# Kernel optimization log

Hardware: AMD Instinct MI355X
Metric: run time of the kernel (lower is better)

Reference implementation:

```python
import jax, jax.numpy as jnp
import numpy as np

B, L, D = 4, 4096, 64

def setup_inputs() -> dict:
    key = jax.random.key(0)
    k1, k2, k3, k4 = jax.random.split(key, 4)
    return {
        "query": jax.random.normal(k1, (B, L, D), dtype=jnp.float32),
        "key": jax.random.normal(k2, (B, L, D), dtype=jnp.float32),
        "value": jax.random.normal(k3, (B, L, D), dtype=jnp.float32),
        "mask": jax.random.uniform(k4, (B, L, L), dtype=jnp.float32),
        "d_k": D,
    }

def reference(query, key, value, mask, d_k):
    # scores: [B, Lq, Lk] = Q @ K^T / sqrt(d_k), then multiplicative mask
    scale = 1.0 / jnp.sqrt(jnp.asarray(d_k, dtype=query.dtype))
    scores = jnp.einsum("bqd,bkd->bqk", query, key) * scale * mask
    attn = jax.nn.softmax(scores, axis=-1)  # row-wise over keys
    return jnp.einsum("bqk,bkd->bqd", attn, value)
```

## Files before the change

kernel.cpp:

```cpp
#include <hip/hip_runtime.h>
#include <hip/hip_bf16.h>
#include <stdint.h>
#include <stddef.h>

#define B_   4
#define L_   4096
#define D_   64
#define TK_  64
#define NKT  (L_/TK_)
#define NKH  (NKT/2)
#define TQ_  64
#define NQB  (L_/TQ_)
#define KROW 144
#define TILE_BYTES (TK_*KROW)

typedef __attribute__((ext_vector_type(8))) short bf16x8;
typedef __attribute__((ext_vector_type(4))) float f32x4;
typedef __attribute__((ext_vector_type(4))) unsigned short u16x4;

__device__ static inline unsigned short f2bf(float x) {
  union { __hip_bfloat16 h; unsigned short u; } cv;
  cv.h = __float2bfloat16(x);
  return cv.u;
}

__global__ __launch_bounds__(512) void attn_fused(
    const float* __restrict__ Q, const float* __restrict__ K,
    const float* __restrict__ V, const float* __restrict__ Mk,
    float* __restrict__ out) {
  __shared__ char Kbuf[2][2][TILE_BYTES];
  __shared__ char Vbuf[2][2][TILE_BYTES];
  __shared__ char Pbuf[8][16*KROW];

  const int idx = blockIdx.x;
  const int b   = (idx & 7) >> 1;
  const int qt  = ((idx >> 3) << 1) | (idx & 1);

  const int tid  = threadIdx.x;
  const int w    = tid >> 6;
  const int qw   = w & 3;
  const int half = w >> 2;
  const int lane = tid & 63;
  const int i16  = lane & 15;
  const int quad = lane >> 4;
  const int q0   = qt*TQ_ + qw*16;

  const int st = tid & 255;
  const int dq = st & 15;
  const int kq = st >> 4;

  const float cs = 0.125f * 1.44269504088896f;
  bf16x8 aq[2];
  {
    const float* qp = Q + ((size_t)b*L_ + q0 + i16)*D_ + quad*8;
#pragma unroll
    for (int ks=0; ks<2; ++ks) {
      const f32x4* p = (const f32x4*)(qp + ks*32);
      f32x4 x0 = p[0], x1 = p[1];
      bf16x8 v;
      for (int j=0;j<4;++j) v[j]   = (short)f2bf(x0[j]*cs);
      for (int j=0;j<4;++j) v[4+j] = (short)f2bf(x1[j]*cs);
      aq[ks] = v;
    }
  }

  const float* mbase = Mk + ((size_t)b*L_ + q0 + quad*4)*(size_t)L_
                          + half*(NKH*TK_) + 4*i16;
  const size_t krow0 = (size_t)b*L_ + (size_t)half*(NKH*TK_) + kq*4;
  const float* kbase = K + krow0*D_ + dq*4;
  const float* vbase = V + krow0*D_ + dq*4;

  f32x4 O[4];
#pragma unroll
  for (int t=0;t<4;++t) O[t] = (f32x4){0.f,0.f,0.f,0.f};
  float l_acc[4] = {0.f,0.f,0.f,0.f};
  f32x4 cmv[4], nmv[4];
  f32x4 kreg[4], vreg[4];

#pragma unroll
  for (int r=0;r<4;++r) {
    kreg[r] = *(const f32x4*)(kbase + (size_t)r*D_);
    vreg[r] = *(const f32x4*)(vbase + (size_t)r*D_);
    cmv[r]  = *(const f32x4*)(mbase + (size_t)r*L_);
  }
#pragma unroll
  for (int r=0;r<4;++r) nmv[r] = cmv[r];

  for (int kt=0; kt<NKH; ++kt) {
    const int buf = kt & 1;

    {
      char* kb = Kbuf[half][buf]; char* vb = Vbuf[half][buf];
#pragma unroll
      for (int r=0;r<4;++r) {
        u16x4 pk;
        for (int j=0;j<4;++j) pk[j] = f2bf(kreg[r][j]);
        *(u16x4*)(kb + (r*16+kq)*KROW + dq*8) = pk;
      }
#pragma unroll
      for (int e=0;e<4;++e) {
        u16x4 pv;
        for (int r=0;r<4;++r) pv[r] = f2bf(vreg[r][e]);
        *(u16x4*)(vb + (dq*4+e)*KROW + kq*8) = pv;
      }
    }
    __syncthreads();

    if (kt+1 < NKH) {
      const size_t roff = (size_t)(kt+1)*TK_*(size_t)D_;
      const size_t kc   = (size_t)(kt+1)*TK_;
#pragma unroll
      for (int r=0;r<4;++r) {
        kreg[r] = *(const f32x4*)(kbase + roff + (size_t)r*D_);
        vreg[r] = *(const f32x4*)(vbase + roff + (size_t)r*D_);
        nmv[r]  = *(const f32x4*)(mbase + (size_t)r*L_ + kc);
      }
    }

    f32x4 acc[4];
    const char* kb = Kbuf[half][buf];
#pragma unroll
    for (int t=0;t<4;++t) {
      acc[t] = (f32x4){0.f,0.f,0.f,0.f};
#pragma unroll
      for (int ks=0;ks<2;++ks) {
        bf16x8 bfr = *(const bf16x8*)(kb + (t*16+i16)*KROW + ks*64 + quad*16);
        acc[t] = __builtin_amdgcn_mfma_f32_16x16x32_bf16(aq[ks], bfr, acc[t], 0,0,0);
      }
    }

    float p[16]; float rs[4] = {0.f,0.f,0.f,0.f};
#pragma unroll
    for (int t=0;t<4;++t)
#pragma unroll
      for (int r=0;r<4;++r) {
        float v = __builtin_amdgcn_exp2f(acc[t][r] * cmv[r][t]);
        p[t*4+r] = v; rs[r] += v;
      }
#pragma unroll
    for (int r=0;r<4;++r) {
      float s = rs[r];
      s += __shfl_xor(s, 1); s += __shfl_xor(s, 2);
      s += __shfl_xor(s, 4); s += __shfl_xor(s, 8);
      l_acc[r] += s;
    }

    char* pb = Pbuf[w];
#pragma unroll
    for (int r=0;r<4;++r) {
      u16x4 pk;
      for (int t=0;t<4;++t) pk[t] = f2bf(p[t*4+r]);
      *(u16x4*)(pb + (quad*4+r)*KROW + i16*8) = pk;
    }

    const char* vb = Vbuf[half][buf];
#pragma unroll
    for (int ks=0;ks<2;++ks) {
      bf16x8 af = *(const bf16x8*)(pb + i16*KROW + ks*64 + quad*16);
#pragma unroll
      for (int dt=0;dt<4;++dt) {
        bf16x8 vf = *(const bf16x8*)(vb + (dt*16+i16)*KROW + ks*64 + quad*16);
        O[dt] = __builtin_amdgcn_mfma_f32_16x16x32_bf16(af, vf, O[dt], 0,0,0);
      }
    }

#pragma unroll
    for (int r=0;r<4;++r) cmv[r] = nmv[r];
  }

  float* Ol = (float*)&Kbuf[0][0][0];
  float* Ll = (float*)&Pbuf[0][0];
  __syncthreads();
  if (half == 1) {
#pragma unroll
    for (int t=0;t<4;++t)
      *(f32x4*)&Ol[((size_t)qw*64 + t*16 + i16)*20 + quad*4] = O[t];
    if (i16 == 0) {
#pragma unroll
      for (int r=0;r<4;++r) Ll[qw*16 + quad*4 + r] = l_acc[r];
    }
  }
  __syncthreads();
  if (half == 0) {
#pragma unroll
    for (int t=0;t<4;++t) {
      f32x4 op = *(const f32x4*)&Ol[((size_t)qw*64 + t*16 + i16)*20 + quad*4];
      O[t] += op;
    }
    float inv[4];
#pragma unroll
    for (int r=0;r<4;++r) inv[r] = 1.0f / (l_acc[r] + Ll[qw*16 + quad*4 + r]);
#pragma unroll
    for (int t=0;t<4;++t)
#pragma unroll
      for (int r=0;r<4;++r)
        out[((size_t)b*L_ + q0 + quad*4 + r)*D_ + t*16 + i16] = O[t][r]*inv[r];
  }
}

extern "C" void kernel_launch(void* const* d_in, const int* in_sizes, int n_in,
                              void* d_out, int out_size, void* d_ws, size_t ws_size,
                              hipStream_t stream) {
  const float* Q  = (const float*)d_in[0];
  const float* K  = (const float*)d_in[1];
  const float* V  = (const float*)d_in[2];
  const float* Mk = (const float*)d_in[3];
  (void)d_ws; (void)ws_size;

  attn_fused<<<B_*NQB, 512, 0, stream>>>(Q, K, V, Mk, (float*)d_out);
}
```

Baseline: 407.5 us.

## Pre-convert K/V to bf16 LDS-layout tiles and compute row sums via MFMA

```diff
diff --git a/kernel.cpp b/kernel.cpp
--- a/kernel.cpp
+++ b/kernel.cpp
@@ -24,10 +24,42 @@
   return cv.u;
 }
 
-__global__ __launch_bounds__(512) void attn_fused(
-    const float* __restrict__ Q, const float* __restrict__ K,
-    const float* __restrict__ V, const float* __restrict__ Mk,
-    float* __restrict__ out) {
+
+__global__ __launch_bounds__(256) void prep_kv(const float* __restrict__ K,
+                                               const float* __restrict__ V,
+                                               char* __restrict__ kws,
+                                               char* __restrict__ vws) {
+  const int blk = blockIdx.x;
+  const int kt  = blk & (NKT-1);
+  const int b   = blk >> 6;
+  const int t   = threadIdx.x;
+  const int kr  = t >> 2;
+  const int ds  = t & 3;
+  const size_t row = (size_t)b*L_ + (size_t)kt*TK_ + kr;
+  const f32x4* kp = (const f32x4*)(K + row*D_ + ds*16);
+  const f32x4* vp = (const f32x4*)(V + row*D_ + ds*16);
+  f32x4 kv[4], vv[4];
+  for (int s=0;s<4;++s){ kv[s]=kp[s]; vv[s]=vp[s]; }
+
+  bf16x8 lo, hi;
+  for (int s=0;s<2;++s) for (int j=0;j<4;++j) lo[s*4+j] = (short)f2bf(kv[s  ][j]);
+  for (int s=0;s<2;++s) for (int j=0;j<4;++j) hi[s*4+j] = (short)f2bf(kv[2+s][j]);
+  const int slot = (kr&3)*16 + (kr>>2);
+  char* kdst = kws + (size_t)blk*TILE_BYTES + slot*KROW + ds*32;
+  *(bf16x8*)(kdst)    = lo;
+  *(bf16x8*)(kdst+16) = hi;
+
+  char* vdst = vws + (size_t)blk*TILE_BYTES + kr*2;
+  for (int s=0;s<4;++s)
+    for (int j=0;j<4;++j)
+      *(unsigned short*)(vdst + (size_t)(ds*16 + s*4 + j)*KROW) = f2bf(vv[s][j]);
+}
+
+__global__ __launch_bounds__(512) void attn_main(const float* __restrict__ Q,
+                                                 const float* __restrict__ Mk,
+                                                 const char* __restrict__ kws,
+                                                 const char* __restrict__ vws,
+                                                 float* __restrict__ out) {
   __shared__ char Kbuf[2][2][TILE_BYTES];
   __shared__ char Vbuf[2][2][TILE_BYTES];
   __shared__ char Pbuf[8][16*KROW];
@@ -45,10 +77,6 @@
   const int quad = lane >> 4;
   const int q0   = qt*TQ_ + qw*16;
 
-  const int st = tid & 255;
-  const int dq = st & 15;
-  const int kq = st >> 4;
-
   const float cs = 0.125f * 1.44269504088896f;
   bf16x8 aq[2];
   {
@@ -64,57 +92,66 @@
     }
   }
 
+  bf16x8 vone;
+#pragma unroll
+  for (int j=0;j<8;++j) vone[j] = (short)0x3F80;
+
   const float* mbase = Mk + ((size_t)b*L_ + q0 + quad*4)*(size_t)L_
                           + half*(NKH*TK_) + 4*i16;
-  const size_t krow0 = (size_t)b*L_ + (size_t)half*(NKH*TK_) + kq*4;
-  const float* kbase = K + krow0*D_ + dq*4;
-  const float* vbase = V + krow0*D_ + dq*4;
 
   f32x4 O[4];
 #pragma unroll
   for (int t=0;t<4;++t) O[t] = (f32x4){0.f,0.f,0.f,0.f};
-  float l_acc[4] = {0.f,0.f,0.f,0.f};
+  f32x4 l4 = (f32x4){0.f,0.f,0.f,0.f};
   f32x4 cmv[4], nmv[4];
-  f32x4 kreg[4], vreg[4];
-
-#pragma unroll
-  for (int r=0;r<4;++r) {
-    kreg[r] = *(const f32x4*)(kbase + (size_t)r*D_);
-    vreg[r] = *(const f32x4*)(vbase + (size_t)r*D_);
-    cmv[r]  = *(const f32x4*)(mbase + (size_t)r*L_);
-  }
+  bf16x8 sreg[5];
+
+  const size_t tb0 = (size_t)(b*NKT + half*NKH)*TILE_BYTES;
+
+#pragma unroll
+  for (int j=0;j<5;++j) {
+    const int c = qw + j*4;
+    if (c < 18) {
+      const char* gsrc = (c < 9)
+          ? (kws + tb0 + (size_t)c*1024)
+          : (vws + tb0 + (size_t)(c-9)*1024);
+      sreg[j] = *(const bf16x8*)(gsrc + lane*16);
+    }
+  }
+#pragma unroll
+  for (int r=0;r<4;++r) cmv[r] = *(const f32x4*)(mbase + (size_t)r*L_);
 #pragma unroll
   for (int r=0;r<4;++r) nmv[r] = cmv[r];
 
   for (int kt=0; kt<NKH; ++kt) {
     const int buf = kt & 1;
 
-    {
-      char* kb = Kbuf[half][buf]; char* vb = Vbuf[half][buf];
-#pragma unroll
-      for (int r=0;r<4;++r) {
-        u16x4 pk;
-        for (int j=0;j<4;++j) pk[j] = f2bf(kreg[r][j]);
-        *(u16x4*)(kb + (r*16+kq)*KROW + dq*8) = pk;
+#pragma unroll
+    for (int j=0;j<5;++j) {
+      const int c = qw + j*4;
+      if (c < 18) {
+        char* ldst = (c < 9) ? &Kbuf[half][buf][c*1024]
+                             : &Vbuf[half][buf][(c-9)*1024];
+        *(bf16x8*)(ldst + lane*16) = sreg[j];
       }
-#pragma unroll
-      for (int e=0;e<4;++e) {
-        u16x4 pv;
-        for (int r=0;r<4;++r) pv[r] = f2bf(vreg[r][e]);
-        *(u16x4*)(vb + (dq*4+e)*KROW + kq*8) = pv;
+    }
+    __syncthreads();
+
+    if (kt+1 < NKH) {
+      const size_t toff = tb0 + (size_t)(kt+1)*TILE_BYTES;
+#pragma unroll
+      for (int j=0;j<5;++j) {
+        const int c = qw + j*4;
+        if (c < 18) {
+          const char* gsrc = (c < 9)
+              ? (kws + toff + (size_t)c*1024)
+              : (vws + toff + (size_t)(c-9)*1024);
+          sreg[j] = *(const bf16x8*)(gsrc + lane*16);
+        }
       }
-    }
-    __syncthreads();
-
-    if (kt+1 < NKH) {
-      const size_t roff = (size_t)(kt+1)*TK_*(size_t)D_;
-      const size_t kc   = (size_t)(kt+1)*TK_;
-#pragma unroll
-      for (int r=0;r<4;++r) {
-        kreg[r] = *(const f32x4*)(kbase + roff + (size_t)r*D_);
-        vreg[r] = *(const f32x4*)(vbase + roff + (size_t)r*D_);
-        nmv[r]  = *(const f32x4*)(mbase + (size_t)r*L_ + kc);
-      }
+      const size_t kc = (size_t)(kt+1)*TK_;
+#pragma unroll
+      for (int r=0;r<4;++r) nmv[r] = *(const f32x4*)(mbase + (size_t)r*L_ + kc);
     }
 
     f32x4 acc[4];
@@ -129,21 +166,12 @@
       }
     }
 
-    float p[16]; float rs[4] = {0.f,0.f,0.f,0.f};
+    float p[16];
 #pragma unroll
     for (int t=0;t<4;++t)
 #pragma unroll
-      for (int r=0;r<4;++r) {
-        float v = __builtin_amdgcn_exp2f(acc[t][r] * cmv[r][t]);
-        p[t*4+r] = v; rs[r] += v;
-      }
-#pragma unroll
-    for (int r=0;r<4;++r) {
-      float s = rs[r];
-      s += __shfl_xor(s, 1); s += __shfl_xor(s, 2);
-      s += __shfl_xor(s, 4); s += __shfl_xor(s, 8);
-      l_acc[r] += s;
-    }
+      for (int r=0;r<4;++r)
+        p[t*4+r] = __builtin_amdgcn_exp2f(acc[t][r] * cmv[r][t]);
 
     char* pb = Pbuf[w];
 #pragma unroll
@@ -154,14 +182,16 @@
     }
 
     const char* vb = Vbuf[half][buf];
-#pragma unroll
-    for (int ks=0;ks<2;++ks) {
-      bf16x8 af = *(const bf16x8*)(pb + i16*KROW + ks*64 + quad*16);
-#pragma unroll
-      for (int dt=0;dt<4;++dt) {
-        bf16x8 vf = *(const bf16x8*)(vb + (dt*16+i16)*KROW + ks*64 + quad*16);
-        O[dt] = __builtin_amdgcn_mfma_f32_16x16x32_bf16(af, vf, O[dt], 0,0,0);
-      }
+    bf16x8 af0 = *(const bf16x8*)(pb + i16*KROW +  0 + quad*16);
+    bf16x8 af1 = *(const bf16x8*)(pb + i16*KROW + 64 + quad*16);
+    l4 = __builtin_amdgcn_mfma_f32_16x16x32_bf16(af0, vone, l4, 0,0,0);
+    l4 = __builtin_amdgcn_mfma_f32_16x16x32_bf16(af1, vone, l4, 0,0,0);
+#pragma unroll
+    for (int dt=0;dt<4;++dt) {
+      bf16x8 vf0 = *(const bf16x8*)(vb + (dt*16+i16)*KROW +  0 + quad*16);
+      O[dt] = __builtin_amdgcn_mfma_f32_16x16x32_bf16(af0, vf0, O[dt], 0,0,0);
+      bf16x8 vf1 = *(const bf16x8*)(vb + (dt*16+i16)*KROW + 64 + quad*16);
+      O[dt] = __builtin_amdgcn_mfma_f32_16x16x32_bf16(af1, vf1, O[dt], 0,0,0);
     }
 
 #pragma unroll
@@ -177,7 +207,7 @@
       *(f32x4*)&Ol[((size_t)qw*64 + t*16 + i16)*20 + quad*4] = O[t];
     if (i16 == 0) {
 #pragma unroll
-      for (int r=0;r<4;++r) Ll[qw*16 + quad*4 + r] = l_acc[r];
+      for (int r=0;r<4;++r) Ll[qw*16 + quad*4 + r] = l4[r];
     }
   }
   __syncthreads();
@@ -189,7 +219,7 @@
     }
     float inv[4];
 #pragma unroll
-    for (int r=0;r<4;++r) inv[r] = 1.0f / (l_acc[r] + Ll[qw*16 + quad*4 + r]);
+    for (int r=0;r<4;++r) inv[r] = 1.0f / (l4[r] + Ll[qw*16 + quad*4 + r]);
 #pragma unroll
     for (int t=0;t<4;++t)
 #pragma unroll
@@ -205,7 +235,10 @@
   const float* K  = (const float*)d_in[1];
   const float* V  = (const float*)d_in[2];
   const float* Mk = (const float*)d_in[3];
-  (void)d_ws; (void)ws_size;
-
-  attn_fused<<<B_*NQB, 512, 0, stream>>>(Q, K, V, Mk, (float*)d_out);
-}
+
+  char* kws = (char*)d_ws;
+  char* vws = kws + (size_t)B_*NKT*TILE_BYTES;
+
+  prep_kv  <<<B_*NKT, 256, 0, stream>>>(K, V, kws, vws);
+  attn_main<<<B_*NQB, 512, 0, stream>>>(Q, Mk, kws, vws, (float*)d_out);
+}
```

New measurement: 389.9 us. -4.3%, faster.
